# Kernel optimization log

Hardware: AMD Instinct MI355X
Metric: run time of the kernel (lower is better)

The kernel has to match this reference:

```python
import jax, jax.numpy as jnp
import numpy as np

NUM_EMBEDDINGS = 1024
EMBEDDING_DIM = 256


def setup_inputs() -> dict:
    key = jax.random.key(0)
    k1, k2 = jax.random.split(key)
    input = jax.random.normal(k1, (64, 32, 32, EMBEDDING_DIM), dtype=jnp.float32)
    weight = jax.random.normal(k2, (NUM_EMBEDDINGS, EMBEDDING_DIM), dtype=jnp.float32)
    return {"input": input, "weight": weight}


def reference(input, weight):
    # Nearest-code lookup: argmin_k 0.5*||mu_k||^2 - <z, mu_k>  (scaled by 2 here,
    # matching torch: sqr - 2*cov). weight: [K, D], input: [..., D].
    sqr = jnp.sum(weight * weight, axis=1)                      # [K]
    cov = jnp.einsum('...j,kj->...k', input, weight)            # [..., K]
    indices = jnp.argmin(sqr - 2.0 * cov, axis=-1)              # [...]
    vectors = jnp.take(weight, indices, axis=0)                 # [..., D]
    # Straight-through estimator: values == vectors, grad flows to input.
    values = jax.lax.stop_gradient(vectors - input) + input
    return values, indices, vectors
```

## Files before the change

kernel.cpp:

```cpp
#include <hip/hip_runtime.h>


constexpr int N_TOK = 65536;
constexpr int KC    = 1024;
constexpr int D     = 256;

constexpr size_t IDX_OFF = (size_t)N_TOK * D;
constexpr size_t VEC_OFF = IDX_OFF + N_TOK;
constexpr int    OWL_CAP = 131072;

#define MARGIN 12.0f

typedef __attribute__((ext_vector_type(8)))  short bf16x8;
typedef __attribute__((ext_vector_type(4)))  float f32x4;
typedef __attribute__((ext_vector_type(16))) float f32x16;

__device__ inline unsigned short f2bf(float x) {
    unsigned int u = __float_as_uint(x);
    unsigned int r = (u + 0x7FFFu + ((u >> 16) & 1u)) >> 16;
    return (unsigned short)r;
}

__device__ inline unsigned int fkey(float f) {
    unsigned int b = __float_as_uint(f);
    return (b & 0x80000000u) ? ~b : (b | 0x80000000u);
}

__global__ __launch_bounds__(64)
void vq_prep(const float* __restrict__ w, unsigned short* __restrict__ wbf,
             float* __restrict__ sqr, int* __restrict__ cnt) {
    const int code = blockIdx.x;
    const int lane = threadIdx.x;
    float4 v = ((const float4*)w)[(size_t)code * 64 + lane];
    float s = v.x * v.x + v.y * v.y + v.z * v.z + v.w * v.w;
#pragma unroll
    for (int off = 32; off >= 1; off >>= 1) s += __shfl_xor(s, off, 64);
    unsigned short* d = wbf + (size_t)code * D + lane * 4;
    d[0] = f2bf(v.x); d[1] = f2bf(v.y); d[2] = f2bf(v.z); d[3] = f2bf(v.w);
    if (lane == 0) sqr[code] = s;
    if (code == 0 && lane == 0) *cnt = 0;
}

constexpr int CT   = 32;
constexpr int NSTG = KC / CT;
constexpr int LCAP = 4096;

struct __align__(16) P1Shared {
    unsigned short sbuf[3][CT * D];
    float sqr[KC];
    int   list[LCAP];
    unsigned long long lcand[128];
    int   lcnt;
};

__device__ __forceinline__ void stage_issue(const char* __restrict__ srcbase,
                                            unsigned short* __restrict__ dstbuf,
                                            const int (&soff)[4], int tid) {
#pragma unroll
    for (int r = 0; r < 4; ++r) {
        __builtin_amdgcn_global_load_lds(
            (const __attribute__((address_space(1))) void*)(srcbase + soff[r]),
            (__attribute__((address_space(3))) void*)(dstbuf + (tid + r * 256) * 8),
            16, 0, 0);
    }
}

template<bool EMIT>
__device__ __forceinline__ void scan(const char* __restrict__ wbfB, P1Shared& sh,
                                     const bf16x8 (&afr)[16], float (&rmin)[16],
                                     int row_base_blk, int wave, int lane,
                                     int cl , int hi ,
                                     int tid, const int (&soff)[4],
                                     int* __restrict__ owl, int* __restrict__ cnt) {
    stage_issue(wbfB, sh.sbuf[0], soff, tid);
    stage_issue(wbfB + 16384, sh.sbuf[1], soff, tid);

    for (int s = 0; s < NSTG; ++s) {
        if (s == NSTG - 1) asm volatile("s_waitcnt vmcnt(0)" ::: "memory");
        else               asm volatile("s_waitcnt vmcnt(4)" ::: "memory");
        __builtin_amdgcn_sched_barrier(0);
        __builtin_amdgcn_s_barrier();
        __builtin_amdgcn_sched_barrier(0);
        if (s + 2 < NSTG)
            stage_issue(wbfB + (s + 2) * 16384, sh.sbuf[(s + 2) % 3], soff, tid);

        const unsigned short* sb = sh.sbuf[s % 3] + (size_t)lane * 8;
        f32x16 acc = {0.f,0.f,0.f,0.f, 0.f,0.f,0.f,0.f,
                      0.f,0.f,0.f,0.f, 0.f,0.f,0.f,0.f};
#pragma unroll
        for (int h = 0; h < 2; ++h) {
            bf16x8 b[8];
#pragma unroll
            for (int kk = 0; kk < 8; ++kk)
                b[kk] = *(const bf16x8*)(sb + (h * 8 + kk) * 512);
#pragma unroll
            for (int kk = 0; kk < 8; ++kk)
                acc = __builtin_amdgcn_mfma_f32_32x32x16_bf16(afr[h * 8 + kk], b[kk], acc, 0, 0, 0);
        }

        const int c0 = s * CT;
        const float sq = sh.sqr[c0 + cl];
#pragma unroll
        for (int r = 0; r < 16; ++r) {
            const float sc = sq - 2.0f * acc[r];
            if (!EMIT) {
                rmin[r] = fminf(rmin[r], sc);
            } else {
                const bool flag = (sc <= rmin[r] + MARGIN);
                unsigned long long mask = __ballot(flag);
                if (mask) {
                    const int leader = __builtin_ctzll(mask);
                    const int nact   = __popcll(mask);
                    const int prefix = __popcll(mask & ((1ULL << lane) - 1ULL));
                    int wbase = 0;
                    if (lane == leader) wbase = atomicAdd(&sh.lcnt, nact);
                    wbase = __shfl(wbase, leader, 64);
                    if (flag) {
                        const int lrow = wave * 32 + (r & 3) + 8 * (r >> 2) + 4 * hi;
                        const int pos  = wbase + prefix;
                        if (pos < LCAP) {
                            sh.list[pos] = (lrow << 10) | (c0 + cl);
                        } else {
                            int g = atomicAdd(cnt, 1);
                            if (g < OWL_CAP)
                                owl[g] = ((row_base_blk + lrow) << 10) | (c0 + cl);
                        }
                    }
                }
            }
        }
    }
}

__global__ __launch_bounds__(256, 1)
void vq_main(const float* __restrict__ input, const float* __restrict__ weight,
             const unsigned short* __restrict__ wbf, const float* __restrict__ sqr,
             int* __restrict__ cnt, int* __restrict__ owl, float* __restrict__ out) {
    __shared__ P1Shared sh;

    const int tid  = threadIdx.x;
    const int wave = tid >> 6;
    const int lane = tid & 63;
    const int cl   = lane & 31;
    const int hi   = lane >> 5;
    const int row_base_blk = blockIdx.x * 128;

    if (tid == 0) sh.lcnt = 0;
    if (tid < 128) sh.lcand[tid] = 0xFFFFFFFFFFFFFFFFULL;
    ((float4*)sh.sqr)[tid] = ((const float4*)sqr)[tid];

    int soff[4];
#pragma unroll
    for (int r = 0; r < 4; ++r) {
        const int sl = tid + r * 256;
        soff[r] = (sl & 31) * 512 + (sl >> 5) * 16;
    }

    bf16x8 afr[16];
    {
        const float* ar = input + (size_t)(row_base_blk + wave * 32 + cl) * D;
#pragma unroll
        for (int kt = 0; kt < 16; ++kt) {
            const int k0 = kt * 16 + hi * 8;
            float4 f0 = *(const float4*)(ar + k0);
            float4 f1 = *(const float4*)(ar + k0 + 4);
            bf16x8 v;
            v[0] = (short)f2bf(f0.x); v[1] = (short)f2bf(f0.y);
            v[2] = (short)f2bf(f0.z); v[3] = (short)f2bf(f0.w);
            v[4] = (short)f2bf(f1.x); v[5] = (short)f2bf(f1.y);
            v[6] = (short)f2bf(f1.z); v[7] = (short)f2bf(f1.w);
            afr[kt] = v;
        }
    }

    float rmin[16];
#pragma unroll
    for (int r = 0; r < 16; ++r) rmin[r] = 3.4e38f;

    __syncthreads();

    scan<false>((const char*)wbf, sh, afr, rmin, row_base_blk, wave, lane,
                cl, hi, tid, soff, owl, cnt);

#pragma unroll
    for (int off = 1; off <= 16; off <<= 1)
#pragma unroll
        for (int r = 0; r < 16; ++r)
            rmin[r] = fminf(rmin[r], __shfl_xor(rmin[r], off, 64));

    __syncthreads();

    scan<true>((const char*)wbf, sh, afr, rmin, row_base_blk, wave, lane,
               cl, hi, tid, soff, owl, cnt);

    __syncthreads();

    {
        const int n  = min(sh.lcnt, LCAP);
        const int sw = tid >> 4;
        const int sl = tid & 15;
        const float4* in4 = (const float4*)input;
        const float4* w4  = (const float4*)weight;
        for (int e = sw; e < n; e += 16) {
            const int ent  = sh.list[e];
            const int lrow = ent >> 10;
            const int code = ent & 1023;
            const float4* zr = in4 + (size_t)(row_base_blk + lrow) * 64;
            const float4* wr = w4 + (size_t)code * 64;
            float s = 0.f;
#pragma unroll
            for (int j = 0; j < 4; ++j) {
                float4 za = zr[sl + 16 * j];
                float4 wa = wr[sl + 16 * j];
                s = fmaf(za.x, wa.x, s);
                s = fmaf(za.y, wa.y, s);
                s = fmaf(za.z, wa.z, s);
                s = fmaf(za.w, wa.w, s);
            }
#pragma unroll
            for (int off = 1; off <= 8; off <<= 1) s += __shfl_xor(s, off, 16);
            if (sl == 0) {
                const float score = sh.sqr[code] - 2.0f * s;
                unsigned long long key =
                    ((unsigned long long)fkey(score) << 32) | (unsigned int)code;
                atomicMin(&sh.lcand[lrow], key);
            }
        }
    }
    __syncthreads();

    if (tid < 128) {
        const int idx = (int)(sh.lcand[tid] & 1023ULL);
        sh.list[tid] = idx;
        out[IDX_OFF + row_base_blk + tid] = (float)idx;
    }
    __syncthreads();
    {
        const float4* w4 = (const float4*)weight;
        float4* out4 = (float4*)out;
        const int q = tid & 63;
#pragma unroll 4
        for (int it = 0; it < 32; ++it) {
            const int lr  = it * 4 + (tid >> 6);
            const int idx = sh.list[lr];
            const size_t grow = (size_t)(row_base_blk + lr);
            float4 v = w4[(size_t)idx * 64 + q];
            out4[grow * 64 + q] = v;
            out4[VEC_OFF / 4 + grow * 64 + q] = v;
        }
    }
}

__global__ __launch_bounds__(256)
void vq_cleanup(const float* __restrict__ input, const float* __restrict__ weight,
                const float* __restrict__ sqr, const int* __restrict__ owl,
                const int* __restrict__ cnt, float* __restrict__ out) {
    const int m = min(*cnt, OWL_CAP);
    if (m == 0) return;
    __shared__ float zrow[D];
    __shared__ unsigned long long best;
    const int tid = threadIdx.x;
    for (int e = blockIdx.x; e < m; e += gridDim.x) {
        const int grow = owl[e] >> 10;
        if (tid == 0) best = 0xFFFFFFFFFFFFFFFFULL;
        if (tid < 64) ((float4*)zrow)[tid] = ((const float4*)input)[(size_t)grow * 64 + tid];
        __syncthreads();
        for (int cc = 0; cc < 4; ++cc) {
            const int code = tid * 4 + cc;
            const float4* wr = (const float4*)weight + (size_t)code * 64;
            float s = 0.f;
            for (int k = 0; k < 64; ++k) {
                float4 wa = wr[k];
                s = fmaf(zrow[4 * k],     wa.x, s);
                s = fmaf(zrow[4 * k + 1], wa.y, s);
                s = fmaf(zrow[4 * k + 2], wa.z, s);
                s = fmaf(zrow[4 * k + 3], wa.w, s);
            }
            const float score = sqr[code] - 2.0f * s;
            unsigned long long key =
                ((unsigned long long)fkey(score) << 32) | (unsigned int)code;
            atomicMin(&best, key);
        }
        __syncthreads();
        const int idx = (int)(best & 1023ULL);
        if (tid == 0) out[IDX_OFF + grow] = (float)idx;
        if (tid < 64) {
            float4 v = ((const float4*)weight)[(size_t)idx * 64 + tid];
            ((float4*)out)[(size_t)grow * 64 + tid] = v;
            ((float4*)out)[VEC_OFF / 4 + (size_t)grow * 64 + tid] = v;
        }
        __syncthreads();
    }
}

extern "C" void kernel_launch(void* const* d_in, const int* in_sizes, int n_in,
                              void* d_out, int out_size, void* d_ws, size_t ws_size,
                              hipStream_t stream) {
    const float* input  = (const float*)d_in[0];
    const float* weight = (const float*)d_in[1];
    float* out = (float*)d_out;

    unsigned short* wbf = (unsigned short*)d_ws;
    float* sqr = (float*)((char*)d_ws + 524288);
    int*   cnt = (int*)((char*)d_ws + 528384);
    int*   owl = (int*)((char*)d_ws + 532480);

    vq_prep   <<<KC, 64, 0, stream>>>(weight, wbf, sqr, cnt);
    vq_main   <<<N_TOK / 128, 256, 0, stream>>>(input, weight, wbf, sqr, cnt, owl, out);
    vq_cleanup<<<64, 256, 0, stream>>>(input, weight, sqr, owl, cnt, out);
}
```

Baseline: 286.9 us.

## Fuse two-pass codebook scan into single pass with running min and split finalize kernel

Replaces the two-pass scan (a full pass to find each row's minimum, then a second pass to emit candidates within a margin) with a single pass. That pass keeps a running row minimum via cross-lane shuffles and emits candidates against it, halving the codebook streaming and MFMA work. Because the running minimum starts loose, more candidates get emitted, so the shared list capacity and the global overflow capacity are raised. The overflow list now lives in the output buffer, and writing the gathered output moves into a separate finish kernel. It also splits the MFMA accumulation into two chains, requests two blocks per CU, and uses more cleanup blocks. The risks are heavy overflow traffic for early stages, extra shuffles in every stage, and lower occupancy than requested given the large LDS footprint.

Result: slower. 402.3 us (+40.2%).

```diff
diff --git a/kernel.cpp b/kernel.cpp
--- a/kernel.cpp
+++ b/kernel.cpp
@@ -7,12 +7,11 @@
 
 constexpr size_t IDX_OFF = (size_t)N_TOK * D;
 constexpr size_t VEC_OFF = IDX_OFF + N_TOK;
-constexpr int    OWL_CAP = 131072;
+constexpr int    OWL_CAP = 1 << 20;
 
 #define MARGIN 12.0f
 
 typedef __attribute__((ext_vector_type(8)))  short bf16x8;
-typedef __attribute__((ext_vector_type(4)))  float f32x4;
 typedef __attribute__((ext_vector_type(16))) float f32x16;
 
 __device__ inline unsigned short f2bf(float x) {
@@ -43,7 +42,7 @@
 
 constexpr int CT   = 32;
 constexpr int NSTG = KC / CT;
-constexpr int LCAP = 4096;
+constexpr int LCAP = 6144;
 
 struct __align__(16) P1Shared {
     unsigned short sbuf[3][CT * D];
@@ -65,77 +64,11 @@
     }
 }
 
-template<bool EMIT>
-__device__ __forceinline__ void scan(const char* __restrict__ wbfB, P1Shared& sh,
-                                     const bf16x8 (&afr)[16], float (&rmin)[16],
-                                     int row_base_blk, int wave, int lane,
-                                     int cl , int hi ,
-                                     int tid, const int (&soff)[4],
-                                     int* __restrict__ owl, int* __restrict__ cnt) {
-    stage_issue(wbfB, sh.sbuf[0], soff, tid);
-    stage_issue(wbfB + 16384, sh.sbuf[1], soff, tid);
-
-    for (int s = 0; s < NSTG; ++s) {
-        if (s == NSTG - 1) asm volatile("s_waitcnt vmcnt(0)" ::: "memory");
-        else               asm volatile("s_waitcnt vmcnt(4)" ::: "memory");
-        __builtin_amdgcn_sched_barrier(0);
-        __builtin_amdgcn_s_barrier();
-        __builtin_amdgcn_sched_barrier(0);
-        if (s + 2 < NSTG)
-            stage_issue(wbfB + (s + 2) * 16384, sh.sbuf[(s + 2) % 3], soff, tid);
-
-        const unsigned short* sb = sh.sbuf[s % 3] + (size_t)lane * 8;
-        f32x16 acc = {0.f,0.f,0.f,0.f, 0.f,0.f,0.f,0.f,
-                      0.f,0.f,0.f,0.f, 0.f,0.f,0.f,0.f};
-#pragma unroll
-        for (int h = 0; h < 2; ++h) {
-            bf16x8 b[8];
-#pragma unroll
-            for (int kk = 0; kk < 8; ++kk)
-                b[kk] = *(const bf16x8*)(sb + (h * 8 + kk) * 512);
-#pragma unroll
-            for (int kk = 0; kk < 8; ++kk)
-                acc = __builtin_amdgcn_mfma_f32_32x32x16_bf16(afr[h * 8 + kk], b[kk], acc, 0, 0, 0);
-        }
-
-        const int c0 = s * CT;
-        const float sq = sh.sqr[c0 + cl];
-#pragma unroll
-        for (int r = 0; r < 16; ++r) {
-            const float sc = sq - 2.0f * acc[r];
-            if (!EMIT) {
-                rmin[r] = fminf(rmin[r], sc);
-            } else {
-                const bool flag = (sc <= rmin[r] + MARGIN);
-                unsigned long long mask = __ballot(flag);
-                if (mask) {
-                    const int leader = __builtin_ctzll(mask);
-                    const int nact   = __popcll(mask);
-                    const int prefix = __popcll(mask & ((1ULL << lane) - 1ULL));
-                    int wbase = 0;
-                    if (lane == leader) wbase = atomicAdd(&sh.lcnt, nact);
-                    wbase = __shfl(wbase, leader, 64);
-                    if (flag) {
-                        const int lrow = wave * 32 + (r & 3) + 8 * (r >> 2) + 4 * hi;
-                        const int pos  = wbase + prefix;
-                        if (pos < LCAP) {
-                            sh.list[pos] = (lrow << 10) | (c0 + cl);
-                        } else {
-                            int g = atomicAdd(cnt, 1);
-                            if (g < OWL_CAP)
-                                owl[g] = ((row_base_blk + lrow) << 10) | (c0 + cl);
-                        }
-                    }
-                }
-            }
-        }
-    }
-}
-
-__global__ __launch_bounds__(256, 1)
-void vq_main(const float* __restrict__ input, const float* __restrict__ weight,
+__global__ __launch_bounds__(256, 2)
+void vq_scan(const float* __restrict__ input, const float* __restrict__ weight,
              const unsigned short* __restrict__ wbf, const float* __restrict__ sqr,
-             int* __restrict__ cnt, int* __restrict__ owl, float* __restrict__ out) {
+             int* __restrict__ cnt, int* __restrict__ owl,
+             unsigned long long* __restrict__ cand) {
     __shared__ P1Shared sh;
 
     const int tid  = threadIdx.x;
@@ -144,6 +77,7 @@
     const int cl   = lane & 31;
     const int hi   = lane >> 5;
     const int row_base_blk = blockIdx.x * 128;
+    const char* wbfB = (const char*)wbf;
 
     if (tid == 0) sh.lcnt = 0;
     if (tid < 128) sh.lcand[tid] = 0xFFFFFFFFFFFFFFFFULL;
@@ -179,19 +113,70 @@
 
     __syncthreads();
 
-    scan<false>((const char*)wbf, sh, afr, rmin, row_base_blk, wave, lane,
-                cl, hi, tid, soff, owl, cnt);
-
-#pragma unroll
-    for (int off = 1; off <= 16; off <<= 1)
-#pragma unroll
-        for (int r = 0; r < 16; ++r)
-            rmin[r] = fminf(rmin[r], __shfl_xor(rmin[r], off, 64));
-
-    __syncthreads();
-
-    scan<true>((const char*)wbf, sh, afr, rmin, row_base_blk, wave, lane,
-               cl, hi, tid, soff, owl, cnt);
+    stage_issue(wbfB, sh.sbuf[0], soff, tid);
+    stage_issue(wbfB + 16384, sh.sbuf[1], soff, tid);
+
+    for (int s = 0; s < NSTG; ++s) {
+        if (s == NSTG - 1) asm volatile("s_waitcnt vmcnt(0)" ::: "memory");
+        else               asm volatile("s_waitcnt vmcnt(4)" ::: "memory");
+        __builtin_amdgcn_sched_barrier(0);
+        __builtin_amdgcn_s_barrier();
+        __builtin_amdgcn_sched_barrier(0);
+        if (s + 2 < NSTG)
+            stage_issue(wbfB + (s + 2) * 16384, sh.sbuf[(s + 2) % 3], soff, tid);
+
+        const unsigned short* sb = sh.sbuf[s % 3] + (size_t)lane * 8;
+        f32x16 acc0 = {0.f,0.f,0.f,0.f, 0.f,0.f,0.f,0.f,
+                       0.f,0.f,0.f,0.f, 0.f,0.f,0.f,0.f};
+        f32x16 acc1 = acc0;
+#pragma unroll
+        for (int h = 0; h < 2; ++h) {
+            bf16x8 b[8];
+#pragma unroll
+            for (int kk = 0; kk < 8; ++kk)
+                b[kk] = *(const bf16x8*)(sb + (h * 8 + kk) * 512);
+#pragma unroll
+            for (int kk = 0; kk < 4; ++kk) {
+                acc0 = __builtin_amdgcn_mfma_f32_32x32x16_bf16(afr[h*8 + 2*kk],     b[2*kk],     acc0, 0, 0, 0);
+                acc1 = __builtin_amdgcn_mfma_f32_32x32x16_bf16(afr[h*8 + 2*kk + 1], b[2*kk + 1], acc1, 0, 0, 0);
+            }
+        }
+
+        const int c0 = s * CT;
+        const float sq = sh.sqr[c0 + cl];
+#pragma unroll
+        for (int r = 0; r < 16; ++r) {
+            const float sc = sq - 2.0f * (acc0[r] + acc1[r]);
+            float m = sc;
+#pragma unroll
+            for (int off = 1; off <= 16; off <<= 1)
+                m = fminf(m, __shfl_xor(m, off, 64));
+            rmin[r] = fminf(rmin[r], m);
+            const bool flag = (sc <= rmin[r] + MARGIN);
+            unsigned long long mask = __ballot(flag);
+            if (mask) {
+                const int leader = __builtin_ctzll(mask);
+                const int nact   = __popcll(mask);
+                const int prefix = __popcll(mask & ((1ULL << lane) - 1ULL));
+                int wbase = 0;
+                if (lane == leader) wbase = atomicAdd(&sh.lcnt, nact);
+                wbase = __shfl(wbase, leader, 64);
+                if (flag) {
+                    const int lrow = wave * 32 + (r & 3) + 8 * (r >> 2) + 4 * hi;
+                    const int pos  = wbase + prefix;
+                    if (pos < LCAP) {
+                        sh.list[pos] = (lrow << 10) | (c0 + cl);
+                    } else {
+                        int g = atomicAdd(cnt, 1);
+                        if (g < OWL_CAP)
+                            owl[g] = ((row_base_blk + lrow) << 10) | (c0 + cl);
+                    }
+                }
+            }
+        }
+        asm volatile("s_waitcnt lgkmcnt(0)" ::: "memory");
+        __builtin_amdgcn_sched_barrier(0);
+    }
 
     __syncthreads();
 
@@ -229,32 +214,13 @@
     }
     __syncthreads();
 
-    if (tid < 128) {
-        const int idx = (int)(sh.lcand[tid] & 1023ULL);
-        sh.list[tid] = idx;
-        out[IDX_OFF + row_base_blk + tid] = (float)idx;
-    }
-    __syncthreads();
-    {
-        const float4* w4 = (const float4*)weight;
-        float4* out4 = (float4*)out;
-        const int q = tid & 63;
-#pragma unroll 4
-        for (int it = 0; it < 32; ++it) {
-            const int lr  = it * 4 + (tid >> 6);
-            const int idx = sh.list[lr];
-            const size_t grow = (size_t)(row_base_blk + lr);
-            float4 v = w4[(size_t)idx * 64 + q];
-            out4[grow * 64 + q] = v;
-            out4[VEC_OFF / 4 + grow * 64 + q] = v;
-        }
-    }
+    if (tid < 128) cand[row_base_blk + tid] = sh.lcand[tid];
 }
 
 __global__ __launch_bounds__(256)
 void vq_cleanup(const float* __restrict__ input, const float* __restrict__ weight,
                 const float* __restrict__ sqr, const int* __restrict__ owl,
-                const int* __restrict__ cnt, float* __restrict__ out) {
+                const int* __restrict__ cnt, unsigned long long* __restrict__ cand) {
     const int m = min(*cnt, OWL_CAP);
     if (m == 0) return;
     __shared__ float zrow[D];
@@ -282,14 +248,34 @@
             atomicMin(&best, key);
         }
         __syncthreads();
-        const int idx = (int)(best & 1023ULL);
-        if (tid == 0) out[IDX_OFF + grow] = (float)idx;
-        if (tid < 64) {
-            float4 v = ((const float4*)weight)[(size_t)idx * 64 + tid];
-            ((float4*)out)[(size_t)grow * 64 + tid] = v;
-            ((float4*)out)[VEC_OFF / 4 + (size_t)grow * 64 + tid] = v;
-        }
+        if (tid == 0) cand[grow] = best;
         __syncthreads();
+    }
+}
+
+__global__ __launch_bounds__(256)
+void vq_finish(const float* __restrict__ weight,
+               const unsigned long long* __restrict__ cand,
+               float* __restrict__ out) {
+    __shared__ int fin[64];
+    const int tid  = threadIdx.x;
+    const int row0 = blockIdx.x * 64;
+    if (tid < 64) {
+        int idx = (int)(cand[row0 + tid] & 1023ULL);
+        fin[tid] = idx;
+        out[IDX_OFF + row0 + tid] = (float)idx;
+    }
+    __syncthreads();
+    const float4* w4 = (const float4*)weight;
+    float4* out4 = (float4*)out;
+#pragma unroll
+    for (int k = 0; k < 16; ++k) {
+        int i = tid + k * 256;
+        int r = i >> 6, q = i & 63;
+        float4 v = w4[(size_t)fin[r] * 64 + q];
+        size_t o = (size_t)(row0 + r) * 64 + q;
+        out4[o] = v;
+        out4[VEC_OFF / 4 + o] = v;
     }
 }
 
@@ -303,9 +289,12 @@
     unsigned short* wbf = (unsigned short*)d_ws;
     float* sqr = (float*)((char*)d_ws + 524288);
     int*   cnt = (int*)((char*)d_ws + 528384);
-    int*   owl = (int*)((char*)d_ws + 532480);
+    unsigned long long* cand = (unsigned long long*)((char*)d_ws + 532480);
+
+    int* owl = (int*)out;
 
     vq_prep   <<<KC, 64, 0, stream>>>(weight, wbf, sqr, cnt);
-    vq_main   <<<N_TOK / 128, 256, 0, stream>>>(input, weight, wbf, sqr, cnt, owl, out);
-    vq_cleanup<<<64, 256, 0, stream>>>(input, weight, sqr, owl, cnt, out);
-}
+    vq_scan   <<<N_TOK / 128, 256, 0, stream>>>(input, weight, wbf, sqr, cnt, owl, cand);
+    vq_cleanup<<<256, 256, 0, stream>>>(input, weight, sqr, owl, cnt, cand);
+    vq_finish <<<N_TOK / 64, 256, 0, stream>>>(weight, cand, out);
+}
```
